# Kernel tuning notes

Hardware: AMD Instinct MI355X
Metric: run time of the kernel (lower is better)

The kernel has to match this reference:

```python
import jax, jax.numpy as jnp
import numpy as np

B = 256
D = 2048          # in_channels (shared latent dim)
S = 8             # n_subjects
OUT = 1000        # sum of 7 Schaefer network head widths [150,148,132,136,76,122,236]


def setup_inputs() -> dict:
    key = jax.random.key(0)
    k1, k2, k3, k4 = jax.random.split(key, 4)
    x = jax.random.normal(k1, (B, D), dtype=jnp.float32)
    subject_ids = jax.random.randint(k2, (B,), 0, S, dtype=jnp.int64)
    scale = 1.0 / np.sqrt(D)  # matches normal_(0, 1/in_channels**0.5)
    # Concatenated per-head weights: equivalent to 7 heads of shapes
    # (S, D, n_k) concatenated along the output axis (n_k sums to OUT).
    W = jax.random.normal(k3, (S, D, OUT), dtype=jnp.float32) * scale
    b = jax.random.normal(k4, (S, OUT), dtype=jnp.float32) * scale
    return {"x": x, "subject_ids": subject_ids, "W": W, "b": b}


def reference(x, subject_ids, W, b):
    # Per-sample weight gather (B, D, OUT) followed by batched matmul,
    # exactly mirroring torch: w = weights[subject_ids]; einsum('bd,bdo->bo').
    w = W[subject_ids]                      # (B, D, OUT) gathered copy
    out = jnp.einsum('bd,bdo->bo', x, w)    # (B, OUT)
    out = out + b[subject_ids]              # per-subject bias
    return out
```

## Files before the change

### kernel.cpp

```cpp
#include <hip/hip_runtime.h>
#include <stdint.h>

#define Bn   256
#define Dn   2048
#define Sn   8
#define ON   1000

#define ROWS 64
#define OT   64
#define KC   512
#define BK   32
#define LDR  40

typedef short v8s __attribute__((ext_vector_type(8)));
typedef float v4f __attribute__((ext_vector_type(4)));

static __device__ __forceinline__ unsigned short f2bf(float f) {
    union { float f; uint32_t u; } v; v.f = f;
    uint32_t u = v.u;
    u += 0x7FFFu + ((u >> 16) & 1u);
    return (unsigned short)(u >> 16);
}

static __device__ __forceinline__ int swz(int row, int g) {
    return (g ^ (row ^ (row >> 3))) & 3;
}

__global__ __launch_bounds__(256) void prep_kernel(const int* __restrict__ sid,
                                                   const float* __restrict__ bias,
                                                   float* __restrict__ out,
                                                   int* __restrict__ perm) {
    const int b = blockIdx.x;
    const int t = threadIdx.x;
    const int s = sid[b];
    for (int o = t; o < ON; o += 256)
        out[b * ON + o] = bias[s * ON + o];

    if (b == 0) {
        __shared__ int cnt[Sn];
        if (t < Sn) cnt[t] = 0;
        perm[t]       = -1;
        perm[t + 256] = -1;
        __syncthreads();
        const int ms  = sid[t];
        const int pos = atomicAdd(&cnt[ms], 1);
        if (pos < ROWS) perm[ms * ROWS + pos] = t;
    }
}

__global__ __launch_bounds__(256) void main_kernel(const float* __restrict__ x,
                                                   const float* __restrict__ W,
                                                   const int* __restrict__ perm,
                                                   float* __restrict__ out) {
    __shared__ unsigned short Ash[ROWS * LDR];
    __shared__ unsigned short Bsh[OT * LDR];
    __shared__ int rows_l[ROWS];

    const int oc = blockIdx.x;
    const int dc = blockIdx.y;
    const int s  = blockIdx.z;
    const int o0 = oc * OT;
    const int d0 = dc * KC;
    const int t  = threadIdx.x;

    if (t < ROWS) rows_l[t] = perm[s * ROWS + t];
    __syncthreads();

    const int lane = t & 63;
    const int wave = t >> 6;
    const int lo16 = lane & 15;
    const int quad = lane >> 4;

    const int arow = t >> 2;
    const int ag   = t & 3;
    const int xrow = rows_l[arow];
    const float* xp = (xrow >= 0) ? (x + (size_t)xrow * Dn + d0 + ag * 8) : x;
    const int aoff = arow * LDR + swz(arow, ag) * 8;

    int og = o0 + (t & 63);
    if (og > ON - 1) og = ON - 1;
    const int brow = t & 63;
    const int bg   = t >> 6;
    const float* wp = W + (size_t)s * Dn * ON + (size_t)(d0 + bg * 8) * ON + og;
    const int boff = brow * LDR + swz(brow, bg) * 8;

    const int ard     = wave * 16 + lo16;
    const int ard_off = ard * LDR + swz(ard, quad) * 8;

    v4f acc[4];
#pragma unroll
    for (int i = 0; i < 4; i++) acc[i] = (v4f){0.f, 0.f, 0.f, 0.f};

    for (int kk = 0; kk < KC; kk += BK) {
        float a0=0.f,a1=0.f,a2=0.f,a3=0.f,a4=0.f,a5=0.f,a6=0.f,a7=0.f;
        if (xrow >= 0) {
            const float4 f0 = *(const float4*)(xp + kk);
            const float4 f1 = *(const float4*)(xp + kk + 4);
            a0=f0.x; a1=f0.y; a2=f0.z; a3=f0.w;
            a4=f1.x; a5=f1.y; a6=f1.z; a7=f1.w;
        }
        v8s av;
        av[0]=(short)f2bf(a0); av[1]=(short)f2bf(a1);
        av[2]=(short)f2bf(a2); av[3]=(short)f2bf(a3);
        av[4]=(short)f2bf(a4); av[5]=(short)f2bf(a5);
        av[6]=(short)f2bf(a6); av[7]=(short)f2bf(a7);
        *(v8s*)&Ash[aoff] = av;

        v8s bv;
#pragma unroll
        for (int j = 0; j < 8; j++)
            bv[j] = (short)f2bf(wp[(size_t)(kk + j) * ON]);
        *(v8s*)&Bsh[boff] = bv;

        __syncthreads();

        const v8s af = *(const v8s*)&Ash[ard_off];
#pragma unroll
        for (int nt = 0; nt < 4; nt++) {
            const int br = nt * 16 + lo16;
            const v8s bf = *(const v8s*)&Bsh[br * LDR + swz(br, quad) * 8];
            acc[nt] = __builtin_amdgcn_mfma_f32_16x16x32_bf16(af, bf, acc[nt], 0, 0, 0);
        }
        __syncthreads();
    }

    const int er0 = wave * 16 + quad * 4;
#pragma unroll
    for (int nt = 0; nt < 4; nt++) {
        const int o = o0 + nt * 16 + lo16;
        if (o < ON) {
#pragma unroll
            for (int r = 0; r < 4; r++) {
                const int bi = rows_l[er0 + r];
                if (bi >= 0) atomicAdd(&out[(size_t)bi * ON + o], acc[nt][r]);
            }
        }
    }
}

extern "C" void kernel_launch(void* const* d_in, const int* in_sizes, int n_in,
                              void* d_out, int out_size, void* d_ws, size_t ws_size,
                              hipStream_t stream) {
    const float* x    = (const float*)d_in[0];
    const int*   sid  = (const int*)d_in[1];
    const float* W    = (const float*)d_in[2];
    const float* bias = (const float*)d_in[3];
    float*       out  = (float*)d_out;
    int*         perm = (int*)d_ws;

    prep_kernel<<<dim3(Bn), dim3(256), 0, stream>>>(sid, bias, out, perm);
    main_kernel<<<dim3(16, 4, 8), dim3(256), 0, stream>>>(x, W, perm, out);
}
```

Baseline: 113.2 us.

## Double-buffer LDS tiles with register prefetch and replace atomics with split-K partial reduction

The main GEMM loop now double-buffers the A and B LDS tiles and prefetches the next K-step's global loads into registers before the barrier, dropping one __syncthreads per iteration. The split-K partial results are written to a workspace buffer, and a new reduce kernel sums them with the bias, replacing global atomicAdd and the bias-initialisation pass. This removes atomic contention and hides load latency, at the cost of an extra kernel launch and a write and read of about 4 MB of partials.

Result: no change. 112.0 us (-1.1%).

```diff
diff --git a/kernel.cpp b/kernel.cpp
--- a/kernel.cpp
+++ b/kernel.cpp
@@ -10,6 +10,8 @@
 #define OT   64
 #define KC   512
 #define BK   32
+#define NITER (KC / BK)
+#define NDC  4
 #define LDR  40
 
 typedef short v8s __attribute__((ext_vector_type(8)));
@@ -27,33 +29,24 @@
 }
 
 __global__ __launch_bounds__(256) void prep_kernel(const int* __restrict__ sid,
-                                                   const float* __restrict__ bias,
-                                                   float* __restrict__ out,
                                                    int* __restrict__ perm) {
-    const int b = blockIdx.x;
     const int t = threadIdx.x;
-    const int s = sid[b];
-    for (int o = t; o < ON; o += 256)
-        out[b * ON + o] = bias[s * ON + o];
-
-    if (b == 0) {
-        __shared__ int cnt[Sn];
-        if (t < Sn) cnt[t] = 0;
-        perm[t]       = -1;
-        perm[t + 256] = -1;
-        __syncthreads();
-        const int ms  = sid[t];
-        const int pos = atomicAdd(&cnt[ms], 1);
-        if (pos < ROWS) perm[ms * ROWS + pos] = t;
-    }
+    __shared__ int cnt[Sn];
+    if (t < Sn) cnt[t] = 0;
+    perm[t]       = -1;
+    perm[t + 256] = -1;
+    __syncthreads();
+    const int ms  = sid[t];
+    const int pos = atomicAdd(&cnt[ms], 1);
+    if (pos < ROWS) perm[ms * ROWS + pos] = t;
 }
 
 __global__ __launch_bounds__(256) void main_kernel(const float* __restrict__ x,
                                                    const float* __restrict__ W,
                                                    const int* __restrict__ perm,
-                                                   float* __restrict__ out) {
-    __shared__ unsigned short Ash[ROWS * LDR];
-    __shared__ unsigned short Bsh[OT * LDR];
+                                                   float* __restrict__ part) {
+    __shared__ unsigned short Ash[2][ROWS * LDR];
+    __shared__ unsigned short Bsh[2][OT * LDR];
     __shared__ int rows_l[ROWS];
 
     const int oc = blockIdx.x;
@@ -91,39 +84,55 @@
 #pragma unroll
     for (int i = 0; i < 4; i++) acc[i] = (v4f){0.f, 0.f, 0.f, 0.f};
 
-    for (int kk = 0; kk < KC; kk += BK) {
-        float a0=0.f,a1=0.f,a2=0.f,a3=0.f,a4=0.f,a5=0.f,a6=0.f,a7=0.f;
-        if (xrow >= 0) {
-            const float4 f0 = *(const float4*)(xp + kk);
-            const float4 f1 = *(const float4*)(xp + kk + 4);
-            a0=f0.x; a1=f0.y; a2=f0.z; a3=f0.w;
-            a4=f1.x; a5=f1.y; a6=f1.z; a7=f1.w;
-        }
+    float4 fa0 = {0.f, 0.f, 0.f, 0.f}, fa1 = {0.f, 0.f, 0.f, 0.f};
+    float fb[8];
+    if (xrow >= 0) {
+        fa0 = *(const float4*)(xp);
+        fa1 = *(const float4*)(xp + 4);
+    }
+#pragma unroll
+    for (int j = 0; j < 8; j++) fb[j] = wp[(size_t)j * ON];
+
+    int cur = 0;
+    for (int it = 0; it < NITER; ++it) {
+        unsigned short* Ab = &Ash[cur][0];
+        unsigned short* Bb = &Bsh[cur][0];
+
         v8s av;
-        av[0]=(short)f2bf(a0); av[1]=(short)f2bf(a1);
-        av[2]=(short)f2bf(a2); av[3]=(short)f2bf(a3);
-        av[4]=(short)f2bf(a4); av[5]=(short)f2bf(a5);
-        av[6]=(short)f2bf(a6); av[7]=(short)f2bf(a7);
-        *(v8s*)&Ash[aoff] = av;
+        av[0]=(short)f2bf(fa0.x); av[1]=(short)f2bf(fa0.y);
+        av[2]=(short)f2bf(fa0.z); av[3]=(short)f2bf(fa0.w);
+        av[4]=(short)f2bf(fa1.x); av[5]=(short)f2bf(fa1.y);
+        av[6]=(short)f2bf(fa1.z); av[7]=(short)f2bf(fa1.w);
+        *(v8s*)&Ab[aoff] = av;
 
         v8s bv;
 #pragma unroll
-        for (int j = 0; j < 8; j++)
-            bv[j] = (short)f2bf(wp[(size_t)(kk + j) * ON]);
-        *(v8s*)&Bsh[boff] = bv;
+        for (int j = 0; j < 8; j++) bv[j] = (short)f2bf(fb[j]);
+        *(v8s*)&Bb[boff] = bv;
+
+        if (it + 1 < NITER) {
+            const int kk = (it + 1) * BK;
+            if (xrow >= 0) {
+                fa0 = *(const float4*)(xp + kk);
+                fa1 = *(const float4*)(xp + kk + 4);
+            }
+#pragma unroll
+            for (int j = 0; j < 8; j++) fb[j] = wp[(size_t)(kk + j) * ON];
+        }
 
         __syncthreads();
 
-        const v8s af = *(const v8s*)&Ash[ard_off];
+        const v8s af = *(const v8s*)&Ab[ard_off];
 #pragma unroll
         for (int nt = 0; nt < 4; nt++) {
             const int br = nt * 16 + lo16;
-            const v8s bf = *(const v8s*)&Bsh[br * LDR + swz(br, quad) * 8];
+            const v8s bf = *(const v8s*)&Bb[br * LDR + swz(br, quad) * 8];
             acc[nt] = __builtin_amdgcn_mfma_f32_16x16x32_bf16(af, bf, acc[nt], 0, 0, 0);
         }
-        __syncthreads();
+        cur ^= 1;
     }
 
+    float* pp = part + (size_t)dc * Bn * ON;
     const int er0 = wave * 16 + quad * 4;
 #pragma unroll
     for (int nt = 0; nt < 4; nt++) {
@@ -132,9 +141,24 @@
 #pragma unroll
             for (int r = 0; r < 4; r++) {
                 const int bi = rows_l[er0 + r];
-                if (bi >= 0) atomicAdd(&out[(size_t)bi * ON + o], acc[nt][r]);
+                if (bi >= 0) pp[(size_t)bi * ON + o] = acc[nt][r];
             }
         }
+    }
+}
+
+__global__ __launch_bounds__(256) void reduce_kernel(const int* __restrict__ sid,
+                                                     const float* __restrict__ bias,
+                                                     const float* __restrict__ part,
+                                                     float* __restrict__ out) {
+    const int b = blockIdx.x;
+    const int s = sid[b];
+    for (int o = threadIdx.x; o < ON; o += 256) {
+        float v = bias[s * ON + o];
+#pragma unroll
+        for (int d = 0; d < NDC; d++)
+            v += part[((size_t)d * Bn + b) * ON + o];
+        out[b * ON + o] = v;
     }
 }
 
@@ -147,7 +171,9 @@
     const float* bias = (const float*)d_in[3];
     float*       out  = (float*)d_out;
     int*         perm = (int*)d_ws;
+    float*       part = (float*)((char*)d_ws + 4096);
 
-    prep_kernel<<<dim3(Bn), dim3(256), 0, stream>>>(sid, bias, out, perm);
-    main_kernel<<<dim3(16, 4, 8), dim3(256), 0, stream>>>(x, W, perm, out);
+    prep_kernel<<<dim3(1), dim3(256), 0, stream>>>(sid, perm);
+    main_kernel<<<dim3(16, NDC, Sn), dim3(256), 0, stream>>>(x, W, perm, part);
+    reduce_kernel<<<dim3(Bn), dim3(256), 0, stream>>>(sid, bias, part, out);
 }
```
